# Performance work log

Hardware: AMD Instinct MI355X
Metric: run time of the kernel (lower is better)

Reference implementation:

```python
import jax, jax.numpy as jnp
import numpy as np

N_NODES = 50000
N_EDGES = 800000
DIM = 64
BN_EPS = 1e-5
L2_EPS = 1e-12


def setup_inputs() -> dict:
    key = jax.random.key(0)
    k1, k2, k3, k4 = jax.random.split(key, 4)
    x = jax.random.normal(k1, (N_NODES, DIM), dtype=jnp.float32)
    edge_index = jax.random.randint(k2, (2, N_EDGES), 0, N_NODES, dtype=jnp.int64)
    W = jax.random.normal(k3, (DIM, DIM), dtype=jnp.float32) * (1.0 / np.sqrt(DIM))
    b = jax.random.normal(k4, (DIM,), dtype=jnp.float32) * 0.02
    gamma = jnp.ones((DIM,), dtype=jnp.float32)
    beta = jnp.zeros((DIM,), dtype=jnp.float32)
    return {"x": x, "edge_index": edge_index, "W": W, "b": b, "gamma": gamma, "beta": beta}


def reference(x, edge_index, W, b, gamma, beta):
    # GCNConv: x' = D^{-1/2} (A + I) D^{-1/2} X W + b  (self-loops added, edge weight 1)
    N = x.shape[0]
    src, dst = edge_index[0], edge_index[1]
    h = x @ W  # [N, dim_out]
    # degree including self-loop
    deg = jnp.ones((N,), x.dtype).at[dst].add(1.0)
    dinv = jax.lax.rsqrt(deg)
    # self-loop contribution: norm_ii = dinv[i]^2
    out = h * (dinv * dinv)[:, None]
    # edge contributions: norm_ij = dinv[src] * dinv[dst], scatter-add to dst
    norm = dinv[src] * dinv[dst]  # [E]
    out = out.at[dst].add(norm[:, None] * h[src])
    out = out + b
    # BatchNorm1d (training mode: biased batch stats)
    mean = out.mean(axis=0)
    var = ((out - mean) ** 2).mean(axis=0)
    out = (out - mean) * jax.lax.rsqrt(var + BN_EPS) * gamma + beta
    # ReLU
    out = jax.nn.relu(out)
    # F.normalize(p=2, dim=1)
    nrm = jnp.sqrt(jnp.sum(out * out, axis=1, keepdims=True))
    out = out / jnp.maximum(nrm, L2_EPS)
    return out
```

## Files before the change

### kernel.cpp

```cpp
#include <hip/hip_runtime.h>

#define DIM 64
#define BN_EPS 1e-5f
#define L2_EPS 1e-12f
#define CAP 64
#define SLOTS 32
#define GBLK 2048
#define FBLK 2048

__global__ __launch_bounds__(256) void k_rg(const int* __restrict__ ei,
                                            int* __restrict__ cur,
                                            unsigned short* __restrict__ es, int E,
                                            const float* __restrict__ x,
                                            const float* __restrict__ W,
                                            float* __restrict__ h, int N) {
    __shared__ float Ws[DIM][DIM];
    __shared__ float xs[16][DIM];
    int bid = blockIdx.x;
    int t = threadIdx.x;
    if ((bid & 3) != 3) {
        int rb = (bid >> 2) * 3 + (bid & 3);
        for (int e = rb * 256 + t; e < E; e += 3072 * 256) {
            int s = ei[e];
            int d = ei[E + e];
            int p = atomicAdd(&cur[d], 1);
            if (p < CAP) es[(size_t)d * CAP + p] = (unsigned short)s;
        }
        return;
    }
    int gb = bid >> 2;
    for (int i = t; i < DIM * DIM; i += 256) Ws[i >> 6][i & 63] = W[i];
    int tx = t & 63, ty = t >> 6;
    const float4* __restrict__ x4 = (const float4*)x;
    for (int r0 = gb * 16; r0 < N; r0 += 1024 * 16) {
        __syncthreads();
        ((float4*)xs)[t] = x4[r0 * 16 + t];
        __syncthreads();
        float a0 = 0.f, a1 = 0.f, a2 = 0.f, a3 = 0.f;
#pragma unroll
        for (int k = 0; k < DIM; ++k) {
            float wv = Ws[k][tx];
            a0 = fmaf(xs[ty][k],      wv, a0);
            a1 = fmaf(xs[ty + 4][k],  wv, a1);
            a2 = fmaf(xs[ty + 8][k],  wv, a2);
            a3 = fmaf(xs[ty + 12][k], wv, a3);
        }
        h[(r0 + ty) * DIM + tx]      = a0;
        h[(r0 + ty + 4) * DIM + tx]  = a1;
        h[(r0 + ty + 8) * DIM + tx]  = a2;
        h[(r0 + ty + 12) * DIM + tx] = a3;
    }
}

__global__ __launch_bounds__(256) void k_gather(const int* __restrict__ cnt,
                                                const unsigned short* __restrict__ es,
                                                const float* __restrict__ h,
                                                const float* __restrict__ b,
                                                float* __restrict__ out,
                                                float* __restrict__ sp, int N) {
    int w = threadIdx.x >> 6;
    int l = threadIdx.x & 63;
    int sub = l >> 4;
    int c = l & 15;
    const float4* __restrict__ h4 = (const float4*)h;
    float4 ss = make_float4(0.f, 0.f, 0.f, 0.f);
    float4 qq = make_float4(0.f, 0.f, 0.f, 0.f);
    for (int d0 = blockIdx.x * 4; d0 < N; d0 += GBLK * 4) {
        int d = d0 + w;
        if (d < N) {
            int deg = min(cnt[d], CAP);
            const unsigned short* __restrict__ row = es + (size_t)d * CAP;
            float4 acc = make_float4(0.f, 0.f, 0.f, 0.f);
            for (int base = 0; base < deg; base += 16) {
#pragma unroll
                for (int u = 0; u < 4; ++u) {
                    int k = base + sub + u * 4;
                    bool valid = k < deg;
                    int s = row[valid ? k : 0];
                    float wgt = valid ? rsqrtf((float)(cnt[s] + 1)) : 0.f;
                    float4 hv = h4[(size_t)s * 16 + c];
                    acc.x = fmaf(wgt, hv.x, acc.x);
                    acc.y = fmaf(wgt, hv.y, acc.y);
                    acc.z = fmaf(wgt, hv.z, acc.z);
                    acc.w = fmaf(wgt, hv.w, acc.w);
                }
            }
            acc.x += __shfl_xor(acc.x, 16, 64); acc.y += __shfl_xor(acc.y, 16, 64);
            acc.z += __shfl_xor(acc.z, 16, 64); acc.w += __shfl_xor(acc.w, 16, 64);
            acc.x += __shfl_xor(acc.x, 32, 64); acc.y += __shfl_xor(acc.y, 32, 64);
            acc.z += __shfl_xor(acc.z, 32, 64); acc.w += __shfl_xor(acc.w, 32, 64);
            if (sub == 0) {
                float dd = rsqrtf((float)(cnt[d] + 1));
                float4 hd = h4[(size_t)d * 16 + c];
                float4 bv = ((const float4*)b)[c];
                float dd2 = dd * dd;
                float4 o;
                o.x = fmaf(dd2, hd.x, fmaf(dd, acc.x, bv.x));
                o.y = fmaf(dd2, hd.y, fmaf(dd, acc.y, bv.y));
                o.z = fmaf(dd2, hd.z, fmaf(dd, acc.z, bv.z));
                o.w = fmaf(dd2, hd.w, fmaf(dd, acc.w, bv.w));
                ((float4*)out)[(size_t)d * 16 + c] = o;
                ss.x += o.x; ss.y += o.y; ss.z += o.z; ss.w += o.w;
                qq.x = fmaf(o.x, o.x, qq.x); qq.y = fmaf(o.y, o.y, qq.y);
                qq.z = fmaf(o.z, o.z, qq.z); qq.w = fmaf(o.w, o.w, qq.w);
            }
        }
    }
    __shared__ float ls[4][DIM], lq[4][DIM];
    if (sub == 0) {
        ls[w][c * 4 + 0] = ss.x; ls[w][c * 4 + 1] = ss.y;
        ls[w][c * 4 + 2] = ss.z; ls[w][c * 4 + 3] = ss.w;
        lq[w][c * 4 + 0] = qq.x; lq[w][c * 4 + 1] = qq.y;
        lq[w][c * 4 + 2] = qq.z; lq[w][c * 4 + 3] = qq.w;
    }
    __syncthreads();
    int t = threadIdx.x;
    if (t < 128) {
        int col = t & 63;
        float v = (t < 64) ? (ls[0][col] + ls[1][col] + ls[2][col] + ls[3][col])
                           : (lq[0][col] + lq[1][col] + lq[2][col] + lq[3][col]);
        atomicAdd(&sp[(blockIdx.x & (SLOTS - 1)) * 128 + t], v);
    }
}

__global__ __launch_bounds__(256) void k_final(float* __restrict__ out,
                                               const float* __restrict__ sp,
                                               const float* __restrict__ gamma,
                                               const float* __restrict__ beta,
                                               int N, float invN) {
    __shared__ float A[DIM], Bc[DIM];
    int t = threadIdx.x;
    if (t < 64) {
        float s = 0.f, q = 0.f;
        for (int k = 0; k < SLOTS; ++k) {
            s += sp[k * 128 + t];
            q += sp[k * 128 + 64 + t];
        }
        float mean = s * invN;
        float var = fmaf(-mean, mean, q * invN);
        float rstd = rsqrtf(var + BN_EPS);
        float a = rstd * gamma[t];
        A[t] = a;
        Bc[t] = fmaf(-mean, a, beta[t]);
    }
    __syncthreads();
    int l = t & 63;
    int w = t >> 6;
    for (int r = blockIdx.x * 4 + w; r < N; r += FBLK * 4) {
        float v = out[r * DIM + l];
        v = fmaf(v, A[l], Bc[l]);
        v = fmaxf(v, 0.f);
        float q = v * v;
#pragma unroll
        for (int off = 32; off; off >>= 1) q += __shfl_xor(q, off, 64);
        float nrm = sqrtf(q);
        out[r * DIM + l] = v / fmaxf(nrm, L2_EPS);
    }
}

extern "C" void kernel_launch(void* const* d_in, const int* in_sizes, int n_in,
                              void* d_out, int out_size, void* d_ws, size_t ws_size,
                              hipStream_t stream) {
    const float* x     = (const float*)d_in[0];
    const int*   ei    = (const int*)d_in[1];
    const float* W     = (const float*)d_in[2];
    const float* b     = (const float*)d_in[3];
    const float* gamma = (const float*)d_in[4];
    const float* beta  = (const float*)d_in[5];
    float* out = (float*)d_out;

    const int N = in_sizes[0] / DIM;
    const int E = in_sizes[1] / 2;

    float* wsf = (float*)d_ws;
    const int SP_OFF  = 0;
    const int CUR_OFF = SLOTS * 128;
    const int H_OFF   = CUR_OFF + ((N + 255) & ~255);
    const int ES_OFF  = H_OFF + N * DIM;

    float* sp  = wsf + SP_OFF;
    int*   cur = (int*)(wsf + CUR_OFF);
    float* h   = wsf + H_OFF;
    unsigned short* es = (unsigned short*)(wsf + ES_OFF);

    hipMemsetAsync(wsf, 0, (size_t)(CUR_OFF + N) * sizeof(float), stream);

    k_rg    <<<4096, 256, 0, stream>>>(ei, cur, es, E, x, W, h, N);
    k_gather<<<GBLK, 256, 0, stream>>>(cur, es, h, b, out, sp, N);
    k_final <<<FBLK, 256, 0, stream>>>(out, sp, gamma, beta, N, 1.0f / N);
}
```

Measured before the change: 170.8 us.

## Fuse all GCN stages into one cooperative persistent kernel with grid syncs

Merges the memset, the bucket/GEMM kernel, the gather kernel and the finalize kernel into a single cooperative launch, with grid.sync between phases. Counters and stat slots are zeroed in-kernel and the grid is sized from an occupancy query. The aim is to remove the memset and the per-launch overhead and gaps between kernels. In exchange the grid is capped at resident blocks (up to 2048), and there are three grid-wide barriers plus cooperative-launch overhead.

```diff
diff --git a/kernel.cpp b/kernel.cpp
--- a/kernel.cpp
+++ b/kernel.cpp
@@ -1,176 +1,183 @@
 #include <hip/hip_runtime.h>
+#include <hip/hip_cooperative_groups.h>
+
+namespace cg = cooperative_groups;
 
 #define DIM 64
 #define BN_EPS 1e-5f
 #define L2_EPS 1e-12f
 #define CAP 64
 #define SLOTS 32
-#define GBLK 2048
-#define FBLK 2048
-
-__global__ __launch_bounds__(256) void k_rg(const int* __restrict__ ei,
-                                            int* __restrict__ cur,
-                                            unsigned short* __restrict__ es, int E,
-                                            const float* __restrict__ x,
-                                            const float* __restrict__ W,
-                                            float* __restrict__ h, int N) {
-    __shared__ float Ws[DIM][DIM];
-    __shared__ float xs[16][DIM];
-    int bid = blockIdx.x;
-    int t = threadIdx.x;
+#define LDS_BYTES 20480
+
+__global__ __launch_bounds__(256, 7) void k_fused(
+        const int* __restrict__ ei, int* __restrict__ cur,
+        unsigned short* __restrict__ es, int E,
+        const float* __restrict__ x, const float* __restrict__ W,
+        float* __restrict__ h, const float* __restrict__ b,
+        const float* __restrict__ gamma, const float* __restrict__ beta,
+        float* __restrict__ out, float* __restrict__ sp, int N, float invN) {
+    cg::grid_group grid = cg::this_grid();
+    extern __shared__ float smem[];
+    const int bid = blockIdx.x, t = threadIdx.x;
+    const int NB = gridDim.x;
+    const int gtid = bid * 256 + t;
+
+    for (int i = gtid; i < N; i += NB * 256) cur[i] = 0;
+    if (gtid < SLOTS * 128) sp[gtid] = 0.f;
+    grid.sync();
+
     if ((bid & 3) != 3) {
         int rb = (bid >> 2) * 3 + (bid & 3);
-        for (int e = rb * 256 + t; e < E; e += 3072 * 256) {
+        const int RB = (NB >> 2) * 3;
+        for (int e = rb * 256 + t; e < E; e += RB * 256) {
             int s = ei[e];
             int d = ei[E + e];
             int p = atomicAdd(&cur[d], 1);
             if (p < CAP) es[(size_t)d * CAP + p] = (unsigned short)s;
         }
-        return;
+    } else {
+        float* Ws = smem;
+        float* xs = smem + DIM * DIM;
+        int gb = bid >> 2;
+        const int GB = NB >> 2;
+        for (int i = t; i < DIM * DIM; i += 256) Ws[i] = W[i];
+        int tx = t & 63, ty = t >> 6;
+        const float4* __restrict__ x4 = (const float4*)x;
+        for (int r0 = gb * 16; r0 < N; r0 += GB * 16) {
+            __syncthreads();
+            ((float4*)xs)[t] = x4[r0 * 16 + t];
+            __syncthreads();
+            float a0 = 0.f, a1 = 0.f, a2 = 0.f, a3 = 0.f;
+#pragma unroll
+            for (int k = 0; k < DIM; ++k) {
+                float wv = Ws[k * DIM + tx];
+                a0 = fmaf(xs[ty * DIM + k],        wv, a0);
+                a1 = fmaf(xs[(ty + 4) * DIM + k],  wv, a1);
+                a2 = fmaf(xs[(ty + 8) * DIM + k],  wv, a2);
+                a3 = fmaf(xs[(ty + 12) * DIM + k], wv, a3);
+            }
+            h[(r0 + ty) * DIM + tx]      = a0;
+            h[(r0 + ty + 4) * DIM + tx]  = a1;
+            h[(r0 + ty + 8) * DIM + tx]  = a2;
+            h[(r0 + ty + 12) * DIM + tx] = a3;
+        }
     }
-    int gb = bid >> 2;
-    for (int i = t; i < DIM * DIM; i += 256) Ws[i >> 6][i & 63] = W[i];
-    int tx = t & 63, ty = t >> 6;
-    const float4* __restrict__ x4 = (const float4*)x;
-    for (int r0 = gb * 16; r0 < N; r0 += 1024 * 16) {
-        __syncthreads();
-        ((float4*)xs)[t] = x4[r0 * 16 + t];
-        __syncthreads();
-        float a0 = 0.f, a1 = 0.f, a2 = 0.f, a3 = 0.f;
+    grid.sync();
+
+    {
+        float* ls = smem;
+        float* lq = smem + 4 * DIM;
+        int w = t >> 6, l = t & 63;
+        int sub = l >> 4, c = l & 15;
+        const float4* __restrict__ h4 = (const float4*)h;
+        float4 ss = make_float4(0.f, 0.f, 0.f, 0.f);
+        float4 qq = make_float4(0.f, 0.f, 0.f, 0.f);
+        for (int d0 = bid * 4; d0 < N; d0 += NB * 4) {
+            int d = d0 + w;
+            if (d < N) {
+                int deg = min(cur[d], CAP);
+                const unsigned short* __restrict__ row = es + (size_t)d * CAP;
+                float4 acc = make_float4(0.f, 0.f, 0.f, 0.f);
+                for (int base = 0; base < deg; base += 16) {
 #pragma unroll
-        for (int k = 0; k < DIM; ++k) {
-            float wv = Ws[k][tx];
-            a0 = fmaf(xs[ty][k],      wv, a0);
-            a1 = fmaf(xs[ty + 4][k],  wv, a1);
-            a2 = fmaf(xs[ty + 8][k],  wv, a2);
-            a3 = fmaf(xs[ty + 12][k], wv, a3);
-        }
-        h[(r0 + ty) * DIM + tx]      = a0;
-        h[(r0 + ty + 4) * DIM + tx]  = a1;
-        h[(r0 + ty + 8) * DIM + tx]  = a2;
-        h[(r0 + ty + 12) * DIM + tx] = a3;
-    }
-}
-
-__global__ __launch_bounds__(256) void k_gather(const int* __restrict__ cnt,
-                                                const unsigned short* __restrict__ es,
-                                                const float* __restrict__ h,
-                                                const float* __restrict__ b,
-                                                float* __restrict__ out,
-                                                float* __restrict__ sp, int N) {
-    int w = threadIdx.x >> 6;
-    int l = threadIdx.x & 63;
-    int sub = l >> 4;
-    int c = l & 15;
-    const float4* __restrict__ h4 = (const float4*)h;
-    float4 ss = make_float4(0.f, 0.f, 0.f, 0.f);
-    float4 qq = make_float4(0.f, 0.f, 0.f, 0.f);
-    for (int d0 = blockIdx.x * 4; d0 < N; d0 += GBLK * 4) {
-        int d = d0 + w;
-        if (d < N) {
-            int deg = min(cnt[d], CAP);
-            const unsigned short* __restrict__ row = es + (size_t)d * CAP;
-            float4 acc = make_float4(0.f, 0.f, 0.f, 0.f);
-            for (int base = 0; base < deg; base += 16) {
-#pragma unroll
-                for (int u = 0; u < 4; ++u) {
-                    int k = base + sub + u * 4;
-                    bool valid = k < deg;
-                    int s = row[valid ? k : 0];
-                    float wgt = valid ? rsqrtf((float)(cnt[s] + 1)) : 0.f;
-                    float4 hv = h4[(size_t)s * 16 + c];
-                    acc.x = fmaf(wgt, hv.x, acc.x);
-                    acc.y = fmaf(wgt, hv.y, acc.y);
-                    acc.z = fmaf(wgt, hv.z, acc.z);
-                    acc.w = fmaf(wgt, hv.w, acc.w);
+                    for (int u = 0; u < 4; ++u) {
+                        int k = base + sub + u * 4;
+                        bool valid = k < deg;
+                        int s = row[valid ? k : 0];
+                        float wgt = valid ? rsqrtf((float)(cur[s] + 1)) : 0.f;
+                        float4 hv = h4[(size_t)s * 16 + c];
+                        acc.x = fmaf(wgt, hv.x, acc.x);
+                        acc.y = fmaf(wgt, hv.y, acc.y);
+                        acc.z = fmaf(wgt, hv.z, acc.z);
+                        acc.w = fmaf(wgt, hv.w, acc.w);
+                    }
+                }
+                acc.x += __shfl_xor(acc.x, 16, 64); acc.y += __shfl_xor(acc.y, 16, 64);
+                acc.z += __shfl_xor(acc.z, 16, 64); acc.w += __shfl_xor(acc.w, 16, 64);
+                acc.x += __shfl_xor(acc.x, 32, 64); acc.y += __shfl_xor(acc.y, 32, 64);
+                acc.z += __shfl_xor(acc.z, 32, 64); acc.w += __shfl_xor(acc.w, 32, 64);
+                if (sub == 0) {
+                    float dd = rsqrtf((float)(cur[d] + 1));
+                    float4 hd = h4[(size_t)d * 16 + c];
+                    float4 bv = ((const float4*)b)[c];
+                    float dd2 = dd * dd;
+                    float4 o;
+                    o.x = fmaf(dd2, hd.x, fmaf(dd, acc.x, bv.x));
+                    o.y = fmaf(dd2, hd.y, fmaf(dd, acc.y, bv.y));
+                    o.z = fmaf(dd2, hd.z, fmaf(dd, acc.z, bv.z));
+                    o.w = fmaf(dd2, hd.w, fmaf(dd, acc.w, bv.w));
+                    ((float4*)out)[(size_t)d * 16 + c] = o;
+                    ss.x += o.x; ss.y += o.y; ss.z += o.z; ss.w += o.w;
+                    qq.x = fmaf(o.x, o.x, qq.x); qq.y = fmaf(o.y, o.y, qq.y);
+                    qq.z = fmaf(o.z, o.z, qq.z); qq.w = fmaf(o.w, o.w, qq.w);
                 }
             }
-            acc.x += __shfl_xor(acc.x, 16, 64); acc.y += __shfl_xor(acc.y, 16, 64);
-            acc.z += __shfl_xor(acc.z, 16, 64); acc.w += __shfl_xor(acc.w, 16, 64);
-            acc.x += __shfl_xor(acc.x, 32, 64); acc.y += __shfl_xor(acc.y, 32, 64);
-            acc.z += __shfl_xor(acc.z, 32, 64); acc.w += __shfl_xor(acc.w, 32, 64);
-            if (sub == 0) {
-                float dd = rsqrtf((float)(cnt[d] + 1));
-                float4 hd = h4[(size_t)d * 16 + c];
-                float4 bv = ((const float4*)b)[c];
-                float dd2 = dd * dd;
-                float4 o;
-                o.x = fmaf(dd2, hd.x, fmaf(dd, acc.x, bv.x));
-                o.y = fmaf(dd2, hd.y, fmaf(dd, acc.y, bv.y));
-                o.z = fmaf(dd2, hd.z, fmaf(dd, acc.z, bv.z));
-                o.w = fmaf(dd2, hd.w, fmaf(dd, acc.w, bv.w));
-                ((float4*)out)[(size_t)d * 16 + c] = o;
-                ss.x += o.x; ss.y += o.y; ss.z += o.z; ss.w += o.w;
-                qq.x = fmaf(o.x, o.x, qq.x); qq.y = fmaf(o.y, o.y, qq.y);
-                qq.z = fmaf(o.z, o.z, qq.z); qq.w = fmaf(o.w, o.w, qq.w);
+        }
+        __syncthreads();
+        if (sub == 0) {
+            ls[w * DIM + c * 4 + 0] = ss.x; ls[w * DIM + c * 4 + 1] = ss.y;
+            ls[w * DIM + c * 4 + 2] = ss.z; ls[w * DIM + c * 4 + 3] = ss.w;
+            lq[w * DIM + c * 4 + 0] = qq.x; lq[w * DIM + c * 4 + 1] = qq.y;
+            lq[w * DIM + c * 4 + 2] = qq.z; lq[w * DIM + c * 4 + 3] = qq.w;
+        }
+        __syncthreads();
+        if (t < 128) {
+            int col = t & 63;
+            float v = (t < 64)
+                ? (ls[col] + ls[DIM + col] + ls[2 * DIM + col] + ls[3 * DIM + col])
+                : (lq[col] + lq[DIM + col] + lq[2 * DIM + col] + lq[3 * DIM + col]);
+            atomicAdd(&sp[(bid & (SLOTS - 1)) * 128 + t], v);
+        }
+    }
+    grid.sync();
+
+    {
+        float* A  = smem;
+        float* Bc = smem + DIM;
+        __syncthreads();
+        if (t < 64) {
+            float s = 0.f, q = 0.f;
+            for (int k = 0; k < SLOTS; ++k) {
+                s += sp[k * 128 + t];
+                q += sp[k * 128 + 64 + t];
             }
-        }
-    }
-    __shared__ float ls[4][DIM], lq[4][DIM];
-    if (sub == 0) {
-        ls[w][c * 4 + 0] = ss.x; ls[w][c * 4 + 1] = ss.y;
-        ls[w][c * 4 + 2] = ss.z; ls[w][c * 4 + 3] = ss.w;
-        lq[w][c * 4 + 0] = qq.x; lq[w][c * 4 + 1] = qq.y;
-        lq[w][c * 4 + 2] = qq.z; lq[w][c * 4 + 3] = qq.w;
-    }
-    __syncthreads();
-    int t = threadIdx.x;
-    if (t < 128) {
-        int col = t & 63;
-        float v = (t < 64) ? (ls[0][col] + ls[1][col] + ls[2][col] + ls[3][col])
-                           : (lq[0][col] + lq[1][col] + lq[2][col] + lq[3][col]);
-        atomicAdd(&sp[(blockIdx.x & (SLOTS - 1)) * 128 + t], v);
-    }
-}
-
-__global__ __launch_bounds__(256) void k_final(float* __restrict__ out,
-                                               const float* __restrict__ sp,
-                                               const float* __restrict__ gamma,
-                                               const float* __restrict__ beta,
-                                               int N, float invN) {
-    __shared__ float A[DIM], Bc[DIM];
-    int t = threadIdx.x;
-    if (t < 64) {
-        float s = 0.f, q = 0.f;
-        for (int k = 0; k < SLOTS; ++k) {
-            s += sp[k * 128 + t];
-            q += sp[k * 128 + 64 + t];
-        }
-        float mean = s * invN;
-        float var = fmaf(-mean, mean, q * invN);
-        float rstd = rsqrtf(var + BN_EPS);
-        float a = rstd * gamma[t];
-        A[t] = a;
-        Bc[t] = fmaf(-mean, a, beta[t]);
-    }
-    __syncthreads();
-    int l = t & 63;
-    int w = t >> 6;
-    for (int r = blockIdx.x * 4 + w; r < N; r += FBLK * 4) {
-        float v = out[r * DIM + l];
-        v = fmaf(v, A[l], Bc[l]);
-        v = fmaxf(v, 0.f);
-        float q = v * v;
+            float mean = s * invN;
+            float var = fmaf(-mean, mean, q * invN);
+            float rstd = rsqrtf(var + BN_EPS);
+            float a = rstd * gamma[t];
+            A[t] = a;
+            Bc[t] = fmaf(-mean, a, beta[t]);
+        }
+        __syncthreads();
+        int l = t & 63, w = t >> 6;
+        for (int r = bid * 4 + w; r < N; r += NB * 4) {
+            float v = out[r * DIM + l];
+            v = fmaf(v, A[l], Bc[l]);
+            v = fmaxf(v, 0.f);
+            float q = v * v;
 #pragma unroll
-        for (int off = 32; off; off >>= 1) q += __shfl_xor(q, off, 64);
-        float nrm = sqrtf(q);
-        out[r * DIM + l] = v / fmaxf(nrm, L2_EPS);
+            for (int off = 32; off; off >>= 1) q += __shfl_xor(q, off, 64);
+            float nrm = sqrtf(q);
+            out[r * DIM + l] = v / fmaxf(nrm, L2_EPS);
+        }
     }
 }
 
 extern "C" void kernel_launch(void* const* d_in, const int* in_sizes, int n_in,
                               void* d_out, int out_size, void* d_ws, size_t ws_size,
                               hipStream_t stream) {
+    const int* ei      = (const int*)d_in[1];
     const float* x     = (const float*)d_in[0];
-    const int*   ei    = (const int*)d_in[1];
     const float* W     = (const float*)d_in[2];
     const float* b     = (const float*)d_in[3];
     const float* gamma = (const float*)d_in[4];
     const float* beta  = (const float*)d_in[5];
     float* out = (float*)d_out;
 
-    const int N = in_sizes[0] / DIM;
-    const int E = in_sizes[1] / 2;
+    int N = in_sizes[0] / DIM;
+    int E = in_sizes[1] / 2;
+    float invN = 1.0f / N;
 
     float* wsf = (float*)d_ws;
     const int SP_OFF  = 0;
@@ -183,9 +190,18 @@
     float* h   = wsf + H_OFF;
     unsigned short* es = (unsigned short*)(wsf + ES_OFF);
 
-    hipMemsetAsync(wsf, 0, (size_t)(CUR_OFF + N) * sizeof(float), stream);
-
-    k_rg    <<<4096, 256, 0, stream>>>(ei, cur, es, E, x, W, h, N);
-    k_gather<<<GBLK, 256, 0, stream>>>(cur, es, h, b, out, sp, N);
-    k_final <<<FBLK, 256, 0, stream>>>(out, sp, gamma, beta, N, 1.0f / N);
+    int maxb = 0;
+    hipOccupancyMaxActiveBlocksPerMultiprocessor(&maxb, (const void*)k_fused, 256, LDS_BYTES);
+    if (maxb < 1) maxb = 1;
+    int nblk = maxb * 256;
+    if (nblk > 2048) nblk = 2048;
+    nblk &= ~3;
+    if (nblk < 4) nblk = 4;
+
+    void* args[] = { (void*)&ei, (void*)&cur, (void*)&es, (void*)&E,
+                     (void*)&x, (void*)&W, (void*)&h, (void*)&b,
+                     (void*)&gamma, (void*)&beta, (void*)&out, (void*)&sp,
+                     (void*)&N, (void*)&invN };
+    hipLaunchCooperativeKernel((const void*)k_fused, dim3(nblk), dim3(256),
+                               args, LDS_BYTES, stream);
 }
```

Measured after the change: 501.3 us. +193.6%, slower.
